# Kernel tuning notes

Measured on AMD Instinct MI355X. Metric: run time of the kernel, lower is better.

The kernel has to match this reference:

```python
import jax, jax.numpy as jnp
import numpy as np

N = 50000
E = 800000
D = 64


def _linear_params(key, d, bias=True):
    kw, kb = jax.random.split(key)
    s = 1.0 / np.sqrt(d)
    W = jax.random.uniform(kw, (d, d), jnp.float32, -s, s)
    if bias:
        b = jax.random.uniform(kb, (d,), jnp.float32, -s, s)
        return W, b
    return W


def setup_inputs() -> dict:
    key = jax.random.key(0)
    ks = jax.random.split(key, 12)
    x_src = jax.random.normal(ks[0], (N, D), jnp.float32)
    x_tgt = jax.random.normal(ks[1], (N, D), jnp.float32)
    t_src = jax.random.normal(ks[2], (N, D), jnp.float32)
    t_tgt = jax.random.normal(ks[3], (N, D), jnp.float32)
    edge_index = jax.random.randint(ks[4], (2, E), 0, N, jnp.int64)
    W_x = _linear_params(ks[5], D, bias=False)
    W_t = _linear_params(ks[6], D, bias=False)
    Ka_W, Ka_b = _linear_params(ks[7], D)
    Qa_W, Qa_b = _linear_params(ks[8], D)
    Kb_W, Kb_b = _linear_params(ks[9], D)
    Qb_W, Qb_b = _linear_params(ks[10], D)
    return dict(x_src=x_src, x_tgt=x_tgt, t_src=t_src, t_tgt=t_tgt,
                edge_index=edge_index, W_x=W_x, W_t=W_t,
                Ka_W=Ka_W, Ka_b=Ka_b, Qa_W=Qa_W, Qa_b=Qa_b,
                Kb_W=Kb_W, Kb_b=Kb_b, Qb_W=Qb_W, Qb_b=Qb_b)


def _segment_softmax(scores, seg, num_segments):
    # numerically stable softmax over edges sharing the same destination node
    m = jax.ops.segment_max(scores, seg, num_segments=num_segments)
    ex = jnp.exp(scores - m[seg])
    denom = jax.ops.segment_sum(ex, seg, num_segments=num_segments)
    return ex / denom[seg]


def reference(x_src, x_tgt, t_src, t_tgt, edge_index,
              W_x, W_t, Ka_W, Ka_b, Qa_W, Qa_b, Kb_W, Kb_b, Qb_W, Qb_b):
    row, col = edge_index[0], edge_index[1]
    n = x_tgt.shape[0]
    d = x_src.shape[-1]
    scale = 1.0 / jnp.sqrt(jnp.float32(d))

    # project on nodes first (cheaper than per-edge), then gather per edge
    q_alpha = (t_tgt @ Qa_W.T + Qa_b)[row]   # [E, D]
    k_alpha = (t_src @ Ka_W.T + Ka_b)[col]
    alpha = _segment_softmax(jnp.sum(q_alpha * k_alpha, -1) * scale, row, n)

    q_beta = (x_tgt @ Qb_W.T + Qb_b)[row]
    k_beta = (x_src @ Kb_W.T + Kb_b)[col]
    beta = _segment_softmax(jnp.sum(q_beta * k_beta, -1) * scale, row, n)

    msg_t = alpha[:, None] * (t_src @ W_t.T)[col]  # [E, D]
    msg_x = beta[:, None] * (x_src @ W_x.T)[col]

    out_x = jax.ops.segment_sum(msg_x, row, num_segments=n)
    out_t = jax.ops.segment_sum(msg_t, row, num_segments=n)
    return out_x, out_t
```

## Files before the change

### kernel.cpp

```cpp
#include <hip/hip_runtime.h>
#include <math.h>


#define D 64
#define NINF -3.0e38f
#define CHUNK 4096
typedef unsigned short ushortT;
typedef unsigned long long ull;
typedef __attribute__((ext_vector_type(8))) short bf16x8;
typedef __attribute__((ext_vector_type(4))) float f32x4;

__device__ __forceinline__ float b2f_lo(unsigned u) {
  return __uint_as_float(u << 16);
}
__device__ __forceinline__ float b2f_hi(unsigned u) {
  return __uint_as_float(u & 0xffff0000u);
}
__device__ __forceinline__ ushortT f2b(float f) {
  unsigned u = __float_as_uint(f);
  u += 0x7fffu + ((u >> 16) & 1u);
  return (ushortT)(u >> 16);
}
__device__ __forceinline__ bf16x8 pack8(float4 v0, float4 v1) {
  bf16x8 r;
  r[0] = (short)f2b(v0.x); r[1] = (short)f2b(v0.y);
  r[2] = (short)f2b(v0.z); r[3] = (short)f2b(v0.w);
  r[4] = (short)f2b(v1.x); r[5] = (short)f2b(v1.y);
  r[6] = (short)f2b(v1.z); r[7] = (short)f2b(v1.w);
  return r;
}

__device__ __forceinline__ bool wave_is64(const ull* __restrict__ ei, ull nNodes) {
  ull v = ei[threadIdx.x & 63];
  return __ballot(v >= nNodes) == 0ull;
}

__global__ __launch_bounds__(256) void pack_hist(
    const void* __restrict__ ei, unsigned* __restrict__ packed,
    int* __restrict__ hist, int E, int N) {
  __shared__ int h[256];
  const int t = threadIdx.x;
  h[t] = 0;
  __syncthreads();
  const bool is64 = wave_is64((const ull*)ei, (ull)N);
  const int base = blockIdx.x * CHUNK + t;
  if (is64) {
    const long long* p = (const long long*)ei;
#pragma unroll 4
    for (int k = 0; k < 16; ++k) {
      int e = base + k * 256;
      if (e < E) {
        unsigned r = (unsigned)(int)p[e];
        unsigned c = (unsigned)(int)p[(long long)E + e];
        packed[e] = (r << 16) | c;
        atomicAdd(&h[r >> 8], 1);
      }
    }
  } else {
    const int* p = (const int*)ei;
#pragma unroll 4
    for (int k = 0; k < 16; ++k) {
      int e = base + k * 256;
      if (e < E) {
        unsigned r = (unsigned)p[e];
        unsigned c = (unsigned)p[E + e];
        packed[e] = (r << 16) | c;
        atomicAdd(&h[r >> 8], 1);
      }
    }
  }
  __syncthreads();
  hist[blockIdx.x * 256 + t] = h[t];
}

__global__ __launch_bounds__(256) void scat_proj(
    const unsigned* __restrict__ packed, const int* __restrict__ hist,
    int* __restrict__ bucketStart, int* __restrict__ offs,
    unsigned* __restrict__ bucketed, int E,
    const float* __restrict__ t_tgt, const float* __restrict__ x_tgt,
    const float* __restrict__ t_src, const float* __restrict__ x_src,
    const float* __restrict__ QaW, const float* __restrict__ Qab_,
    const float* __restrict__ QbW, const float* __restrict__ Qbb,
    const float* __restrict__ KaW, const float* __restrict__ Kab_,
    const float* __restrict__ Wt,
    const float* __restrict__ KbW, const float* __restrict__ Kbb,
    const float* __restrict__ Wx,
    float* __restrict__ qab, ushortT* __restrict__ kab, ushortT* __restrict__ vtx,
    int N, int bpj, int scatBlocks, int nE) {
  const int tid = threadIdx.x;

  if (blockIdx.x < scatBlocks) {
    __shared__ int baseA[256];
    __shared__ int cnt[256];
    __shared__ int scT[256];
    const int b = blockIdx.x;
    int pre = 0, tot = 0;
    for (int i = 0; i < scatBlocks; ++i) {
      int v = hist[i * 256 + tid];
      if (i < b) pre += v;
      tot += v;
    }
    scT[tid] = tot;
    __syncthreads();
    for (int off = 1; off < 256; off <<= 1) {
      int add = (tid >= off) ? scT[tid - off] : 0;
      __syncthreads();
      scT[tid] += add;
      __syncthreads();
    }
    const int bstart = scT[tid] - tot;
    baseA[tid] = bstart + pre;
    cnt[tid] = 0;
    if (b == 0) {
      bucketStart[tid] = bstart;
      if (tid == 0) {
        bucketStart[256] = nE;
        offs[N] = nE;
      }
    }
    __syncthreads();
    const int base = b * CHUNK + tid;
#pragma unroll 4
    for (int k = 0; k < 16; ++k) {
      int e = base + k * 256;
      if (e < E) {
        unsigned v = packed[e];
        int bin = v >> 24;
        int dst = baseA[bin] + atomicAdd(&cnt[bin], 1);
        bucketed[dst] = v;
      }
    }
    return;
  }

  const int tile = blockIdx.x - scatBlocks;
  const int job = tile / bpj;
  const int jb = tile % bpj;
  const float *X, *W0, *B0, *W1 = nullptr;
  switch (job) {
    case 0: X = t_tgt; W0 = QaW; B0 = Qab_; break;
    case 1: X = x_tgt; W0 = QbW; B0 = Qbb; break;
    case 2: X = t_src; W0 = KaW; B0 = Kab_; W1 = Wt; break;
    default: X = x_src; W0 = KbW; B0 = Kbb; W1 = Wx; break;
  }
  const bool dual = (job >= 2);
  const int half = (job & 1) ? 64 : 0;
  const int base = jb * 128;

  const int lane = tid & 63;
  const int wid = tid >> 6;
  const int m16 = lane & 15;
  const int quad = lane >> 4;

  f32x4 acc0[2][4], acc1[2][4];
#pragma unroll
  for (int mt = 0; mt < 2; ++mt)
#pragma unroll
    for (int nt = 0; nt < 4; ++nt) {
      acc0[mt][nt] = (f32x4){0.f, 0.f, 0.f, 0.f};
      acc1[mt][nt] = (f32x4){0.f, 0.f, 0.f, 0.f};
    }

#pragma unroll
  for (int ko = 0; ko < 2; ++ko) {
    const int koff = ko * 32 + quad * 8;
    bf16x8 a[2];
#pragma unroll
    for (int mt = 0; mt < 2; ++mt) {
      const int gnode = base + wid * 32 + mt * 16 + m16;
      float4 v0 = make_float4(0.f, 0.f, 0.f, 0.f), v1 = v0;
      if (gnode < N) {
        const float* p = X + (size_t)gnode * D + koff;
        v0 = *(const float4*)p;
        v1 = *(const float4*)(p + 4);
      }
      a[mt] = pack8(v0, v1);
    }
#pragma unroll
    for (int nt = 0; nt < 4; ++nt) {
      const float* pw = W0 + (nt * 16 + m16) * D + koff;
      bf16x8 bfr = pack8(*(const float4*)pw, *(const float4*)(pw + 4));
#pragma unroll
      for (int mt = 0; mt < 2; ++mt)
        acc0[mt][nt] = __builtin_amdgcn_mfma_f32_16x16x32_bf16(
            a[mt], bfr, acc0[mt][nt], 0, 0, 0);
    }
    if (dual) {
#pragma unroll
      for (int nt = 0; nt < 4; ++nt) {
        const float* pw = W1 + (nt * 16 + m16) * D + koff;
        bf16x8 bfr = pack8(*(const float4*)pw, *(const float4*)(pw + 4));
#pragma unroll
        for (int mt = 0; mt < 2; ++mt)
          acc1[mt][nt] = __builtin_amdgcn_mfma_f32_16x16x32_bf16(
              a[mt], bfr, acc1[mt][nt], 0, 0, 0);
      }
    }
  }

  float bias[4];
#pragma unroll
  for (int nt = 0; nt < 4; ++nt) bias[nt] = B0[nt * 16 + m16];
#pragma unroll
  for (int mt = 0; mt < 2; ++mt) {
#pragma unroll
    for (int reg = 0; reg < 4; ++reg) {
      int node = base + wid * 32 + mt * 16 + quad * 4 + reg;
      if (node < N) {
        if (!dual) {
          float* dst = qab + (size_t)node * 128 + half;
#pragma unroll
          for (int nt = 0; nt < 4; ++nt)
            dst[nt * 16 + m16] = acc0[mt][nt][reg] + bias[nt];
        } else {
          ushortT* dk = kab + (size_t)node * 128 + half;
          ushortT* dv = vtx + (size_t)node * 128 + half;
#pragma unroll
          for (int nt = 0; nt < 4; ++nt) {
            dk[nt * 16 + m16] = f2b(acc0[mt][nt][reg] + bias[nt]);
            dv[nt * 16 + m16] = f2b(acc1[mt][nt][reg]);
          }
        }
      }
    }
  }
}

__global__ __launch_bounds__(256) void build_csr(
    const unsigned* __restrict__ bucketed, const int* __restrict__ bucketStart,
    int* __restrict__ offs, ushortT* __restrict__ ecol, int N) {
  __shared__ int cnt[256], sc[256], cnt2[256];
  __shared__ ushortT lcol[8192];
  const int t = threadIdx.x;
  const int b = blockIdx.x;
  const int start = bucketStart[b];
  int nb = bucketStart[b + 1] - start;
  if (nb > 8192) nb = 8192;
  cnt[t] = 0;
  cnt2[t] = 0;
  __syncthreads();
  for (int i = t; i < nb; i += 256)
    atomicAdd(&cnt[(bucketed[start + i] >> 16) & 255], 1);
  __syncthreads();
  const int c = cnt[t];
  sc[t] = c;
  __syncthreads();
  for (int off = 1; off < 256; off <<= 1) {
    int add = (t >= off) ? sc[t - off] : 0;
    __syncthreads();
    sc[t] += add;
    __syncthreads();
  }
  const int loffs_t = sc[t] - c;
  sc[t] = loffs_t;
  const int row = b * 256 + t;
  if (row < N) offs[row] = start + loffs_t;
  __syncthreads();
  for (int i = t; i < nb; i += 256) {
    unsigned v = bucketed[start + i];
    int r = (v >> 16) & 255;
    int pos = sc[r] + atomicAdd(&cnt2[r], 1);
    lcol[pos] = (ushortT)(v & 0xFFFFu);
  }
  __syncthreads();
  for (int i = t; i < nb; i += 256) ecol[start + i] = lcol[i];
}

__global__ __launch_bounds__(256) void node_attn(
    const float* __restrict__ qab, const ushortT* __restrict__ kab,
    const ushortT* __restrict__ vtx,
    const int* __restrict__ offs, const ushortT* __restrict__ ecol,
    float* __restrict__ out_x, float* __restrict__ out_t, int nNodes) {
  const int lane = threadIdx.x & 63;
  const int sub = lane >> 4;
  const int sl = lane & 15;
  const int gw = (blockIdx.x * blockDim.x + threadIdx.x) >> 6;
  const int nw = (gridDim.x * blockDim.x) >> 6;
  const float scale = 0.125f;

  for (int n = gw; n < nNodes; n += nw) {
    const int s = offs[n];
    const int dg = offs[n + 1] - s;
    const size_t nb = (size_t)n * D;
    if (dg == 0) {
      out_t[nb + lane] = 0.f;
      out_x[nb + lane] = 0.f;
      continue;
    }
    const float4 q0 = *(const float4*)(qab + (size_t)n * 128 + sl * 8);
    const float4 q1 = *(const float4*)(qab + (size_t)n * 128 + sl * 8 + 4);

    float m = NINF, d = 0.f;
    float acc[8];
#pragma unroll
    for (int j = 0; j < 8; ++j) acc[j] = 0.f;

    for (int i = 0; i < dg; i += 8) {
      const int i0 = i + sub;
      const int i1 = i + 4 + sub;
      const bool a0 = i0 < dg, a1 = i1 < dg;
      const int c0 = (int)ecol[s + (a0 ? i0 : 0)];
      const int c1 = (int)ecol[s + (a1 ? i1 : 0)];
      const uint4 k0 = *(const uint4*)(kab + (size_t)c0 * 128 + sl * 8);
      const uint4 v0 = *(const uint4*)(vtx + (size_t)c0 * 128 + sl * 8);
      const uint4 k1 = *(const uint4*)(kab + (size_t)c1 * 128 + sl * 8);
      const uint4 v1 = *(const uint4*)(vtx + (size_t)c1 * 128 + sl * 8);

      {
        float t = q0.x * b2f_lo(k0.x);
        t = fmaf(q0.y, b2f_hi(k0.x), t);
        t = fmaf(q0.z, b2f_lo(k0.y), t);
        t = fmaf(q0.w, b2f_hi(k0.y), t);
        t = fmaf(q1.x, b2f_lo(k0.z), t);
        t = fmaf(q1.y, b2f_hi(k0.z), t);
        t = fmaf(q1.z, b2f_lo(k0.w), t);
        t = fmaf(q1.w, b2f_hi(k0.w), t);
#pragma unroll
        for (int off = 1; off < 8; off <<= 1) t += __shfl_xor(t, off);
        const float sc = a0 ? t * scale : NINF;
        const float mN = fmaxf(m, sc);
        const float f = __expf(m - mN);
        const float w = a0 ? __expf(sc - mN) : 0.f;
        d = d * f + w;
        acc[0] = fmaf(acc[0], f, w * b2f_lo(v0.x));
        acc[1] = fmaf(acc[1], f, w * b2f_hi(v0.x));
        acc[2] = fmaf(acc[2], f, w * b2f_lo(v0.y));
        acc[3] = fmaf(acc[3], f, w * b2f_hi(v0.y));
        acc[4] = fmaf(acc[4], f, w * b2f_lo(v0.z));
        acc[5] = fmaf(acc[5], f, w * b2f_hi(v0.z));
        acc[6] = fmaf(acc[6], f, w * b2f_lo(v0.w));
        acc[7] = fmaf(acc[7], f, w * b2f_hi(v0.w));
        m = mN;
      }
      {
        float t = q0.x * b2f_lo(k1.x);
        t = fmaf(q0.y, b2f_hi(k1.x), t);
        t = fmaf(q0.z, b2f_lo(k1.y), t);
        t = fmaf(q0.w, b2f_hi(k1.y), t);
        t = fmaf(q1.x, b2f_lo(k1.z), t);
        t = fmaf(q1.y, b2f_hi(k1.z), t);
        t = fmaf(q1.z, b2f_lo(k1.w), t);
        t = fmaf(q1.w, b2f_hi(k1.w), t);
#pragma unroll
        for (int off = 1; off < 8; off <<= 1) t += __shfl_xor(t, off);
        const float sc = a1 ? t * scale : NINF;
        const float mN = fmaxf(m, sc);
        const float f = __expf(m - mN);
        const float w = a1 ? __expf(sc - mN) : 0.f;
        d = d * f + w;
        acc[0] = fmaf(acc[0], f, w * b2f_lo(v1.x));
        acc[1] = fmaf(acc[1], f, w * b2f_hi(v1.x));
        acc[2] = fmaf(acc[2], f, w * b2f_lo(v1.y));
        acc[3] = fmaf(acc[3], f, w * b2f_hi(v1.y));
        acc[4] = fmaf(acc[4], f, w * b2f_lo(v1.z));
        acc[5] = fmaf(acc[5], f, w * b2f_hi(v1.z));
        acc[6] = fmaf(acc[6], f, w * b2f_lo(v1.w));
        acc[7] = fmaf(acc[7], f, w * b2f_hi(v1.w));
        m = mN;
      }
    }

    float mg = m;
#pragma unroll
    for (int off = 16; off < 64; off <<= 1) mg = fmaxf(mg, __shfl_xor(mg, off));
    const float fg = __expf(m - mg);
    d *= fg;
#pragma unroll
    for (int j = 0; j < 8; ++j) acc[j] *= fg;
#pragma unroll
    for (int off = 16; off < 64; off <<= 1) {
      d += __shfl_xor(d, off);
#pragma unroll
      for (int j = 0; j < 8; ++j) acc[j] += __shfl_xor(acc[j], off);
    }
    const float inv = 1.0f / d;
    if (sub == 0) {
      float4 o0, o1;
      o0.x = acc[0] * inv; o0.y = acc[1] * inv;
      o0.z = acc[2] * inv; o0.w = acc[3] * inv;
      o1.x = acc[4] * inv; o1.y = acc[5] * inv;
      o1.z = acc[6] * inv; o1.w = acc[7] * inv;
      float* dst = (sl < 8) ? (out_t + nb + sl * 8) : (out_x + nb + (sl - 8) * 8);
      *(float4*)dst = o0;
      *(float4*)(dst + 4) = o1;
    }
  }
}

extern "C" void kernel_launch(void* const* d_in, const int* in_sizes, int n_in,
                              void* d_out, int out_size, void* d_ws, size_t ws_size,
                              hipStream_t stream) {
  const float* x_src = (const float*)d_in[0];
  const float* x_tgt = (const float*)d_in[1];
  const float* t_src = (const float*)d_in[2];
  const float* t_tgt = (const float*)d_in[3];
  const void* edge_index = d_in[4];
  const float* W_x = (const float*)d_in[5];
  const float* W_t = (const float*)d_in[6];
  const float* Ka_W = (const float*)d_in[7];
  const float* Ka_b = (const float*)d_in[8];
  const float* Qa_W = (const float*)d_in[9];
  const float* Qa_b = (const float*)d_in[10];
  const float* Kb_W = (const float*)d_in[11];
  const float* Kb_b = (const float*)d_in[12];
  const float* Qb_W = (const float*)d_in[13];
  const float* Qb_b = (const float*)d_in[14];

  const int N = in_sizes[0] / D;
  const int E = in_sizes[4] / 2;

  char* ws = (char*)d_ws;
  size_t ofs = 0;
  auto carve = [&](size_t bytes) {
    size_t p = ofs;
    ofs += (bytes + 255) & ~(size_t)255;
    return p;
  };
  float* qab = (float*)(ws + carve((size_t)N * 128 * 4));
  ushortT* kab = (ushortT*)(ws + carve((size_t)N * 128 * 2));
  ushortT* vtx = (ushortT*)(ws + carve((size_t)N * 128 * 2));
  unsigned* packed = (unsigned*)(ws + carve((size_t)E * 4));
  unsigned* bucketed = (unsigned*)(ws + carve((size_t)E * 4));
  ushortT* ecol = (ushortT*)(ws + carve((size_t)E * 2));
  const int nBlocks = (E + CHUNK - 1) / CHUNK;
  int* hist = (int*)(ws + carve((size_t)nBlocks * 256 * 4));
  int* bucketStart = (int*)(ws + carve(257 * 4));
  int* offs = (int*)(ws + carve(((size_t)N + 1) * 4));
  (void)ws_size;

  float* out_x = (float*)d_out;
  float* out_t = out_x + (size_t)N * D;

  const int bpj = (N + 127) / 128;
  const int projBlocks = 4 * bpj;

  pack_hist<<<nBlocks, 256, 0, stream>>>(edge_index, packed, hist, E, N);
  scat_proj<<<nBlocks + projBlocks, 256, 0, stream>>>(
      packed, hist, bucketStart, offs, bucketed, E,
      t_tgt, x_tgt, t_src, x_src,
      Qa_W, Qa_b, Qb_W, Qb_b,
      Ka_W, Ka_b, W_t,
      Kb_W, Kb_b, W_x,
      qab, kab, vtx, N, bpj, nBlocks, E);
  build_csr<<<256, 256, 0, stream>>>(bucketed, bucketStart, offs, ecol, N);
  node_attn<<<(N + 3) / 4, 256, 0, stream>>>(qab, kab, vtx, offs, ecol,
                                             out_x, out_t, N);
}
```

Before: 233.8 us.

## Drop packed edge buffer and stage bucket scatter through shared memory

The histogram pass now reads only the row indices and no longer writes a packed edge array. The scatter blocks re-read the edge index directly, do a local counting sort of their chunk into LDS, then write each bucket out as contiguous runs. This removes a global write and re-read of the packed array and makes the scattered writes to the bucketed buffer more contiguous. In exchange it adds a second edge-index read, about 16 KB of extra LDS per block (which may lower occupancy for the projection blocks sharing the kernel), and an extra block-wide scan.

Result: faster. 228.5 us (-2.2%).

```diff
diff --git a/kernel.cpp b/kernel.cpp
--- a/kernel.cpp
+++ b/kernel.cpp
@@ -36,8 +36,7 @@
 }
 
 __global__ __launch_bounds__(256) void pack_hist(
-    const void* __restrict__ ei, unsigned* __restrict__ packed,
-    int* __restrict__ hist, int E, int N) {
+    const void* __restrict__ ei, int* __restrict__ hist, int E, int N) {
   __shared__ int h[256];
   const int t = threadIdx.x;
   h[t] = 0;
@@ -49,24 +48,14 @@
 #pragma unroll 4
     for (int k = 0; k < 16; ++k) {
       int e = base + k * 256;
-      if (e < E) {
-        unsigned r = (unsigned)(int)p[e];
-        unsigned c = (unsigned)(int)p[(long long)E + e];
-        packed[e] = (r << 16) | c;
-        atomicAdd(&h[r >> 8], 1);
-      }
+      if (e < E) atomicAdd(&h[((unsigned)(int)p[e]) >> 8], 1);
     }
   } else {
     const int* p = (const int*)ei;
 #pragma unroll 4
     for (int k = 0; k < 16; ++k) {
       int e = base + k * 256;
-      if (e < E) {
-        unsigned r = (unsigned)p[e];
-        unsigned c = (unsigned)p[E + e];
-        packed[e] = (r << 16) | c;
-        atomicAdd(&h[r >> 8], 1);
-      }
+      if (e < E) atomicAdd(&h[((unsigned)p[e]) >> 8], 1);
     }
   }
   __syncthreads();
@@ -74,7 +63,7 @@
 }
 
 __global__ __launch_bounds__(256) void scat_proj(
-    const unsigned* __restrict__ packed, const int* __restrict__ hist,
+    const void* __restrict__ ei, const int* __restrict__ hist,
     int* __restrict__ bucketStart, int* __restrict__ offs,
     unsigned* __restrict__ bucketed, int E,
     const float* __restrict__ t_tgt, const float* __restrict__ x_tgt,
@@ -86,13 +75,16 @@
     const float* __restrict__ KbW, const float* __restrict__ Kbb,
     const float* __restrict__ Wx,
     float* __restrict__ qab, ushortT* __restrict__ kab, ushortT* __restrict__ vtx,
-    int N, int bpj, int scatBlocks, int nE) {
+    int N, int bpj, int scatBlocks) {
   const int tid = threadIdx.x;
 
   if (blockIdx.x < scatBlocks) {
     __shared__ int baseA[256];
     __shared__ int cnt[256];
+    __shared__ int lofs[256];
+    __shared__ int cnt2[256];
     __shared__ int scT[256];
+    __shared__ unsigned lpack[CHUNK];
     const int b = blockIdx.x;
     int pre = 0, tot = 0;
     for (int i = 0; i < scatBlocks; ++i) {
@@ -111,24 +103,65 @@
     const int bstart = scT[tid] - tot;
     baseA[tid] = bstart + pre;
     cnt[tid] = 0;
+    cnt2[tid] = 0;
     if (b == 0) {
       bucketStart[tid] = bstart;
       if (tid == 0) {
-        bucketStart[256] = nE;
-        offs[N] = nE;
-      }
-    }
-    __syncthreads();
+        bucketStart[256] = E;
+        offs[N] = E;
+      }
+    }
+    __syncthreads();
+    const bool is64 = wave_is64((const ull*)ei, (ull)N);
+    int r[16], c[16];
     const int base = b * CHUNK + tid;
-#pragma unroll 4
+    if (is64) {
+      const long long* p = (const long long*)ei;
+#pragma unroll
+      for (int k = 0; k < 16; ++k) {
+        int e = base + k * 256;
+        r[k] = (e < E) ? (int)p[e] : -1;
+        c[k] = (e < E) ? (int)p[(long long)E + e] : 0;
+      }
+    } else {
+      const int* p = (const int*)ei;
+#pragma unroll
+      for (int k = 0; k < 16; ++k) {
+        int e = base + k * 256;
+        r[k] = (e < E) ? p[e] : -1;
+        c[k] = (e < E) ? p[E + e] : 0;
+      }
+    }
+#pragma unroll
+    for (int k = 0; k < 16; ++k)
+      if (r[k] >= 0) atomicAdd(&cnt[r[k] >> 8], 1);
+    __syncthreads();
+    const int cv = cnt[tid];
+    scT[tid] = cv;
+    __syncthreads();
+    for (int off = 1; off < 256; off <<= 1) {
+      int add = (tid >= off) ? scT[tid - off] : 0;
+      __syncthreads();
+      scT[tid] += add;
+      __syncthreads();
+    }
+    lofs[tid] = scT[tid] - cv;
+    __syncthreads();
+#pragma unroll
     for (int k = 0; k < 16; ++k) {
-      int e = base + k * 256;
-      if (e < E) {
-        unsigned v = packed[e];
-        int bin = v >> 24;
-        int dst = baseA[bin] + atomicAdd(&cnt[bin], 1);
-        bucketed[dst] = v;
-      }
+      if (r[k] >= 0) {
+        int bin = r[k] >> 8;
+        int kk = atomicAdd(&cnt2[bin], 1);
+        lpack[lofs[bin] + kk] = ((unsigned)r[k] << 16) | (unsigned)c[k];
+      }
+    }
+    __syncthreads();
+    const int rem = E - b * CHUNK;
+    const int nblk = rem < CHUNK ? rem : CHUNK;
+    for (int i = tid; i < nblk; i += 256) {
+      unsigned v = lpack[i];
+      int bin = v >> 24;
+      bucketed[baseA[bin] + (i - lofs[bin])] = v;
     }
     return;
   }
@@ -419,7 +452,6 @@
   float* qab = (float*)(ws + carve((size_t)N * 128 * 4));
   ushortT* kab = (ushortT*)(ws + carve((size_t)N * 128 * 2));
   ushortT* vtx = (ushortT*)(ws + carve((size_t)N * 128 * 2));
-  unsigned* packed = (unsigned*)(ws + carve((size_t)E * 4));
   unsigned* bucketed = (unsigned*)(ws + carve((size_t)E * 4));
   ushortT* ecol = (ushortT*)(ws + carve((size_t)E * 2));
   const int nBlocks = (E + CHUNK - 1) / CHUNK;
@@ -434,14 +466,14 @@
   const int bpj = (N + 127) / 128;
   const int projBlocks = 4 * bpj;
 
-  pack_hist<<<nBlocks, 256, 0, stream>>>(edge_index, packed, hist, E, N);
+  pack_hist<<<nBlocks, 256, 0, stream>>>(edge_index, hist, E, N);
   scat_proj<<<nBlocks + projBlocks, 256, 0, stream>>>(
-      packed, hist, bucketStart, offs, bucketed, E,
+      edge_index, hist, bucketStart, offs, bucketed, E,
       t_tgt, x_tgt, t_src, x_src,
       Qa_W, Qa_b, Qb_W, Qb_b,
       Ka_W, Ka_b, W_t,
       Kb_W, Kb_b, W_x,
-      qab, kab, vtx, N, bpj, nBlocks, E);
+      qab, kab, vtx, N, bpj, nBlocks);
   build_csr<<<256, 256, 0, stream>>>(bucketed, bucketStart, offs, ecol, N);
   node_attn<<<(N + 3) / 4, 256, 0, stream>>>(qab, kab, vtx, offs, ecol,
                                              out_x, out_t, N);
```
